# Kernel optimization log

Hardware: AMD Instinct MI355X
Metric: run time of the kernel (lower is better)

## Reference

```python
import jax, jax.numpy as jnp
import numpy as np

N, E, B = 100000, 1200000, 512
IN_DIM, HID, K, NCLS = 64, 64, 3, 10


def setup_inputs() -> dict:
    key = jax.random.key(0)
    ks = jax.random.split(key, 10)
    features = jax.random.normal(ks[0], (N, IN_DIM), jnp.float32)
    edge_src = jax.random.randint(ks[1], (E,), 0, N)
    edge_dst = jax.random.randint(ks[2], (E,), 0, N)
    graph_ids = jnp.sort(jax.random.randint(ks[3], (N,), 0, B))
    s1 = float(1.0 / np.sqrt(IN_DIM))
    W1 = jax.random.uniform(ks[4], (IN_DIM, HID), jnp.float32, -s1, s1)
    b1 = jnp.zeros((HID,), jnp.float32)
    s2 = float(1.0 / np.sqrt(HID))
    W2 = jax.random.uniform(ks[5], (HID, HID), jnp.float32, -s2, s2)
    b2 = jnp.zeros((HID,), jnp.float32)
    s3 = float(1.0 / np.sqrt(HID * 3))
    cw = jax.random.uniform(ks[6], (HID, HID, 3), jnp.float32, -s3, s3)
    cb = jax.random.uniform(ks[7], (HID,), jnp.float32, -s3, s3)
    Wc = jax.random.uniform(ks[8], (HID, NCLS), jnp.float32, -s2, s2)
    bc = jax.random.uniform(ks[9], (NCLS,), jnp.float32, -s2, s2)
    return dict(features=features, edge_src=edge_src, edge_dst=edge_dst,
                graph_ids=graph_ids, num_graphs=B,
                W1=W1, b1=b1, W2=W2, b2=b2, cw=cw, cb=cb, Wc=Wc, bc=bc)


def graph_conv(h, src, dst, W, b, n_nodes):
    # DGL GraphConv, norm='both', allow_zero_in_degree (degrees clamped to 1)
    ones = jnp.ones((src.shape[0],), h.dtype)
    out_deg = jnp.zeros((n_nodes,), h.dtype).at[src].add(ones)
    in_deg = jnp.zeros((n_nodes,), h.dtype).at[dst].add(ones)
    norm_s = jax.lax.rsqrt(jnp.clip(out_deg, 1.0, None))
    norm_d = jax.lax.rsqrt(jnp.clip(in_deg, 1.0, None))
    m = (h * norm_s[:, None]) @ W  # weight first; math identical to agg-first
    agg = jnp.zeros((n_nodes, W.shape[1]), h.dtype).at[dst].add(m[src])
    return agg * norm_d[:, None] + b


def sort_pool(h, gid, num_graphs, k):
    # DGL SortPooling: sort each node's features ascending along feature dim,
    # then take top-k nodes per graph by last feature value (descending),
    # zero-padding graphs with < k nodes. Output [num_graphs, k*D].
    hs = jnp.sort(h, axis=-1)
    key = hs[:, -1]
    order = jnp.lexsort((-key, gid))  # gid asc, key desc
    gid_s = gid[order]
    hs_s = hs[order]
    n = gid.shape[0]
    start = jnp.full((num_graphs,), n).at[gid_s].min(jnp.arange(n))
    rank = jnp.arange(n) - start[gid_s]  # within-graph rank by key desc
    mask = rank < k
    slot = gid_s * k + jnp.clip(rank, 0, k - 1)
    out = jnp.zeros((num_graphs * k, hs.shape[-1]), h.dtype).at[slot].add(
        jnp.where(mask[:, None], hs_s, jnp.zeros((), h.dtype)))
    return out.reshape(num_graphs, k * hs.shape[-1])


def reference(features, edge_src, edge_dst, graph_ids, num_graphs,
              W1, b1, W2, b2, cw, cb, Wc, bc):
    n = features.shape[0]
    h = jax.nn.relu(graph_conv(features, edge_src, edge_dst, W1, b1, n))
    h = jax.nn.relu(graph_conv(h, edge_src, edge_dst, W2, b2, n))
    p = sort_pool(h, graph_ids, num_graphs, K)          # [B, K*HID]
    x = p.reshape(num_graphs, HID, K)                    # faithful torch reshape
    # Conv1d(kernel=3, stride=1) on length-3 input -> length-1 output
    y = jax.nn.relu(jnp.einsum('bct,oct->bo', x, cw) + cb)
    return y @ Wc + bc
```

## Files before the change

### kernel.cpp

```cpp
#include <hip/hip_runtime.h>
#include <hip/hip_bf16.h>


#define PART_H 25088
#define HALF_H (PART_H / 2)
#define PART_F 12544
#define QUART_F (PART_F / 4)
#define MCH  64

__global__ void __launch_bounds__(256) k_histgemm(
    const int* __restrict__ esrc, const int* __restrict__ edst,
    unsigned char* __restrict__ hd, unsigned char* __restrict__ hs,
    const float* __restrict__ in, const float* __restrict__ W,
    float* __restrict__ mout, int N, int E, int PH, int histBlocks) {
  __shared__ float smem[12800];
  const int t = threadIdx.x;
  if (blockIdx.x < histBlocks) {
    unsigned int* lc = (unsigned int*)smem;
    const int b = blockIdx.x;
    const int half = PH * MCH;
    const int a = b / half;
    const int r = b % half;
    const int p = r % PH;
    const int m = r / PH;
    const int* __restrict__ arr = a ? esrc : edst;
    unsigned char* __restrict__ outp = a ? hs : hd;
    const int base = p * PART_H;
    const int lim = min(PART_H, N - base);
    for (int i = t; i < HALF_H; i += 256) lc[i] = 0u;
    __syncthreads();
    const long long cb = (long long)m * E / MCH;
    const long long ce = (long long)(m + 1) * E / MCH;
    const long long a0 = min((cb + 3) & ~3LL, ce);
    const long long nv = (ce - a0) >> 2;
    for (long long e = cb + t; e < a0; e += 256) {
      int d = arr[e] - base;
      if ((unsigned)d < (unsigned)lim) atomicAdd(&lc[d >> 1], 1u << ((d & 1) * 16));
    }
    const int4* __restrict__ a4p = (const int4*)(arr + a0);
    for (long long i = t; i < nv; i += 256) {
      int4 v4 = a4p[i];
      int d;
      d = v4.x - base; if ((unsigned)d < (unsigned)lim) atomicAdd(&lc[d >> 1], 1u << ((d & 1) * 16));
      d = v4.y - base; if ((unsigned)d < (unsigned)lim) atomicAdd(&lc[d >> 1], 1u << ((d & 1) * 16));
      d = v4.z - base; if ((unsigned)d < (unsigned)lim) atomicAdd(&lc[d >> 1], 1u << ((d & 1) * 16));
      d = v4.w - base; if ((unsigned)d < (unsigned)lim) atomicAdd(&lc[d >> 1], 1u << ((d & 1) * 16));
    }
    for (long long e = a0 + (nv << 2) + t; e < ce; e += 256) {
      int d = arr[e] - base;
      if ((unsigned)d < (unsigned)lim) atomicAdd(&lc[d >> 1], 1u << ((d & 1) * 16));
    }
    __syncthreads();
    unsigned char* slice = outp + ((size_t)p * MCH + m) * PART_H;
    for (int i = t; i < lim; i += 256)
      slice[i] = (unsigned char)((lc[i >> 1] >> ((i & 1) * 16)) & 0xffffu);
  } else {
    float* Wl = smem;
    float* Ac = smem + 4096;
    const int ch = (t & 7) * 8;
    const int nb = (t >> 3) * 4;
    for (int i = t; i < 1024; i += 256)
      ((float4*)Wl)[i] = ((const float4*)W)[i];
    const int gb = blockIdx.x - histBlocks;
    const int ng = gridDim.x - histBlocks;
    const int NT = (N + 127) >> 7;
    for (int tile = gb; tile < NT; tile += ng) {
      const int vbase = tile << 7;
      __syncthreads();
      for (int i = t; i < 2048; i += 256) {
        const int r = i >> 4;
        const int c = (i & 15) * 4;
        const int v = vbase + r;
        float4 val = make_float4(0.f, 0.f, 0.f, 0.f);
        if (v < N) val = *(const float4*)(in + (size_t)v * 64 + c);
        Ac[(c + 0) * 136 + r] = val.x;
        Ac[(c + 1) * 136 + r] = val.y;
        Ac[(c + 2) * 136 + r] = val.z;
        Ac[(c + 3) * 136 + r] = val.w;
      }
      __syncthreads();
      float acc[4][8];
#pragma unroll
      for (int j = 0; j < 4; ++j)
#pragma unroll
        for (int c = 0; c < 8; ++c) acc[j][c] = 0.f;
      for (int k = 0; k < 64; k += 4) {
#pragma unroll
        for (int kk = 0; kk < 4; ++kk) {
          const float4 aa = *(const float4*)&Ac[(k + kk) * 136 + nb];
          const float4 w0 = *(const float4*)&Wl[(k + kk) * 64 + ch];
          const float4 w1 = *(const float4*)&Wl[(k + kk) * 64 + ch + 4];
          const float an[4] = {aa.x, aa.y, aa.z, aa.w};
          const float wn[8] = {w0.x, w0.y, w0.z, w0.w, w1.x, w1.y, w1.z, w1.w};
#pragma unroll
          for (int j = 0; j < 4; ++j)
#pragma unroll
            for (int c = 0; c < 8; ++c)
              acc[j][c] = fmaf(an[j], wn[c], acc[j][c]);
        }
      }
#pragma unroll
      for (int j = 0; j < 4; ++j) {
        const int v = vbase + nb + j;
        if (v < N) {
          float4 o0, o1;
          o0.x = acc[j][0]; o0.y = acc[j][1]; o0.z = acc[j][2]; o0.w = acc[j][3];
          o1.x = acc[j][4]; o1.y = acc[j][5]; o1.z = acc[j][6]; o1.w = acc[j][7];
          *(float4*)(mout + (size_t)v * 64 + ch)     = o0;
          *(float4*)(mout + (size_t)v * 64 + ch + 4) = o1;
        }
      }
    }
  }
}

__global__ void k_off(unsigned char* __restrict__ hd, const unsigned char* __restrict__ hs,
                      int* __restrict__ deg_d, float* __restrict__ norm_s,
                      float* __restrict__ norm_d, int N) {
  int v = blockIdx.x * blockDim.x + threadIdx.x;
  if (v >= N) return;
  size_t base = (size_t)(v / PART_H) * MCH * PART_H + (v % PART_H);
  int run = 0;
#pragma unroll
  for (int m = 0; m < MCH; ++m) {
    int t = hd[base + (size_t)m * PART_H];
    hd[base + (size_t)m * PART_H] = (unsigned char)run;
    run += t;
  }
  int s = 0;
#pragma unroll
  for (int m = 0; m < MCH; ++m) s += hs[base + (size_t)m * PART_H];
  deg_d[v] = run;
  norm_d[v] = rsqrtf((float)max(run, 1));
  norm_s[v] = rsqrtf((float)max(s, 1));
}

__global__ void k_scan1(const int* __restrict__ deg, int* __restrict__ rowptr,
                        int* __restrict__ bsum, int N) {
  __shared__ int sums[256];
  const int t = threadIdx.x;
  const int base = blockIdx.x * 2048 + t * 8;
  int loc[8];
  int tot = 0;
#pragma unroll
  for (int j = 0; j < 8; ++j) {
    int idx = base + j;
    loc[j] = tot;
    tot += (idx < N) ? deg[idx] : 0;
  }
  sums[t] = tot;
  __syncthreads();
  for (int off = 1; off < 256; off <<= 1) {
    int x = (t >= off) ? sums[t - off] : 0;
    __syncthreads();
    sums[t] += x;
    __syncthreads();
  }
  int excl = (t == 0) ? 0 : sums[t - 1];
#pragma unroll
  for (int j = 0; j < 8; ++j) {
    int idx = base + j;
    if (idx < N) rowptr[idx] = excl + loc[j];
  }
  if (t == 255) bsum[blockIdx.x] = sums[255];
}

__global__ void k_scan2(int* __restrict__ bsum, int nb) {
  int lane = threadIdx.x;
  int v = (lane < nb) ? bsum[lane] : 0;
  int inc = v;
#pragma unroll
  for (int off = 1; off < 64; off <<= 1) {
    int o = __shfl_up(inc, off, 64);
    if (lane >= off) inc += o;
  }
  if (lane < nb) bsum[lane] = inc - v;
}

__global__ void k_scan3(int* __restrict__ rowptr, const int* __restrict__ bsum, int N) {
  int v = blockIdx.x * blockDim.x + threadIdx.x;
  if (v < N) rowptr[v] += bsum[v >> 11];
}

__global__ void k_fill2(const int* __restrict__ esrc, const int* __restrict__ edst,
                        const unsigned char* __restrict__ hd, const int* __restrict__ rowptr,
                        int* __restrict__ csr, int N, int E, int PF) {
  __shared__ unsigned int cur4[QUART_F];
  const int b = blockIdx.x;
  const int p = b % PF;
  const int m = b / PF;
  const int base = p * PART_F;
  const int lim = min(PART_F, N - base);
  const unsigned char* slice = hd + ((size_t)(p >> 1) * MCH + m) * PART_H
                                  + (size_t)(p & 1) * PART_F;
  const unsigned int* slice4 = (const unsigned int*)slice;
  for (int i = threadIdx.x; i < QUART_F; i += blockDim.x) cur4[i] = slice4[i];
  __syncthreads();
  const int* __restrict__ rp = rowptr + base;
  const long long cb = (long long)m * E / MCH;
  const long long ce = (long long)(m + 1) * E / MCH;
  const long long a0 = min((cb + 3) & ~3LL, ce);
  const long long nv = (ce - a0) >> 2;
  for (long long e = cb + threadIdx.x; e < a0; e += blockDim.x) {
    int d = edst[e] - base;
    if ((unsigned)d < (unsigned)lim) {
      unsigned int old = atomicAdd(&cur4[d >> 2], 1u << ((d & 3) * 8));
      csr[rp[d] + ((old >> ((d & 3) * 8)) & 0xff)] = esrc[e];
    }
  }
  const int4* __restrict__ d4p = (const int4*)(edst + a0);
  const int4* __restrict__ s4p = (const int4*)(esrc + a0);
  for (long long i = threadIdx.x; i < nv; i += blockDim.x) {
    int4 d4 = d4p[i];
    int4 s4 = s4p[i];
    int d;
    d = d4.x - base;
    if ((unsigned)d < (unsigned)lim) {
      unsigned int old = atomicAdd(&cur4[d >> 2], 1u << ((d & 3) * 8));
      csr[rp[d] + ((old >> ((d & 3) * 8)) & 0xff)] = s4.x;
    }
    d = d4.y - base;
    if ((unsigned)d < (unsigned)lim) {
      unsigned int old = atomicAdd(&cur4[d >> 2], 1u << ((d & 3) * 8));
      csr[rp[d] + ((old >> ((d & 3) * 8)) & 0xff)] = s4.y;
    }
    d = d4.z - base;
    if ((unsigned)d < (unsigned)lim) {
      unsigned int old = atomicAdd(&cur4[d >> 2], 1u << ((d & 3) * 8));
      csr[rp[d] + ((old >> ((d & 3) * 8)) & 0xff)] = s4.z;
    }
    d = d4.w - base;
    if ((unsigned)d < (unsigned)lim) {
      unsigned int old = atomicAdd(&cur4[d >> 2], 1u << ((d & 3) * 8));
      csr[rp[d] + ((old >> ((d & 3) * 8)) & 0xff)] = s4.w;
    }
  }
  for (long long e = a0 + (nv << 2) + threadIdx.x; e < ce; e += blockDim.x) {
    int d = edst[e] - base;
    if ((unsigned)d < (unsigned)lim) {
      unsigned int old = atomicAdd(&cur4[d >> 2], 1u << ((d & 3) * 8));
      csr[rp[d] + ((old >> ((d & 3) * 8)) & 0xff)] = esrc[e];
    }
  }
}

__global__ void __launch_bounds__(256) k_gemm64(
    const float* __restrict__ in, const float* __restrict__ norm,
    const float* __restrict__ W, float* __restrict__ out, int N) {
  __shared__ float Wl[4096];
  __shared__ float Ac[64 * 136];
  const int t = threadIdx.x;
  const int ch = (t & 7) * 8;
  const int nb = (t >> 3) * 4;
  for (int i = t; i < 1024; i += 256)
    ((float4*)Wl)[i] = ((const float4*)W)[i];
  const int NT = (N + 127) >> 7;
  for (int tile = blockIdx.x; tile < NT; tile += gridDim.x) {
    const int vbase = tile << 7;
    __syncthreads();
    for (int i = t; i < 2048; i += 256) {
      const int r = i >> 4;
      const int c = (i & 15) * 4;
      const int v = vbase + r;
      float4 val = make_float4(0.f, 0.f, 0.f, 0.f);
      if (v < N) val = *(const float4*)(in + (size_t)v * 64 + c);
      Ac[(c + 0) * 136 + r] = val.x;
      Ac[(c + 1) * 136 + r] = val.y;
      Ac[(c + 2) * 136 + r] = val.z;
      Ac[(c + 3) * 136 + r] = val.w;
    }
    __syncthreads();
    float acc[4][8];
#pragma unroll
    for (int j = 0; j < 4; ++j)
#pragma unroll
      for (int c = 0; c < 8; ++c) acc[j][c] = 0.f;
    for (int k = 0; k < 64; k += 4) {
#pragma unroll
      for (int kk = 0; kk < 4; ++kk) {
        const float4 aa = *(const float4*)&Ac[(k + kk) * 136 + nb];
        const float4 w0 = *(const float4*)&Wl[(k + kk) * 64 + ch];
        const float4 w1 = *(const float4*)&Wl[(k + kk) * 64 + ch + 4];
        const float an[4] = {aa.x, aa.y, aa.z, aa.w};
        const float wn[8] = {w0.x, w0.y, w0.z, w0.w, w1.x, w1.y, w1.z, w1.w};
#pragma unroll
        for (int j = 0; j < 4; ++j)
#pragma unroll
          for (int c = 0; c < 8; ++c)
            acc[j][c] = fmaf(an[j], wn[c], acc[j][c]);
      }
    }
#pragma unroll
    for (int j = 0; j < 4; ++j) {
      const int v = vbase + nb + j;
      if (v < N) {
        const float nm = norm[v];
        float4 o0, o1;
        o0.x = acc[j][0] * nm; o0.y = acc[j][1] * nm;
        o0.z = acc[j][2] * nm; o0.w = acc[j][3] * nm;
        o1.x = acc[j][4] * nm; o1.y = acc[j][5] * nm;
        o1.z = acc[j][6] * nm; o1.w = acc[j][7] * nm;
        *(float4*)(out + (size_t)v * 64 + ch)     = o0;
        *(float4*)(out + (size_t)v * 64 + ch + 4) = o1;
      }
    }
  }
}

__global__ void k_gather(const float* __restrict__ m, const int* __restrict__ rowptr,
                         const int* __restrict__ deg, const float* __restrict__ norm_d,
                         const float* __restrict__ bias, const int* __restrict__ csr,
                         const float* __restrict__ nsrc,
                         const int* __restrict__ gid, int* __restrict__ gstart,
                         float* __restrict__ h, float* __restrict__ key, int N) {
  const int w = blockIdx.x * (blockDim.x >> 6) + (threadIdx.x >> 6);
  if (w >= N) return;
  const int lane = threadIdx.x & 63;
  const int quad = lane & 15;
  const int grp = lane >> 4;
  if (gid != nullptr && lane == 0) {
    int g = gid[w];
    if (w == 0 || gid[w - 1] != g) gstart[g] = w;
  }
  const int start = rowptr[w];
  const int cnt = deg[w];
  float4 acc0 = make_float4(0.f, 0.f, 0.f, 0.f);
  float4 acc1 = make_float4(0.f, 0.f, 0.f, 0.f);
  int i = grp;
  if (nsrc != nullptr) {
    for (; i + 4 < cnt; i += 8) {
      int s0 = csr[start + i];
      int s1 = csr[start + i + 4];
      float n0 = nsrc[s0], n1 = nsrc[s1];
      const float4 v0 = *(const float4*)(m + (size_t)s0 * 64 + quad * 4);
      const float4 v1 = *(const float4*)(m + (size_t)s1 * 64 + quad * 4);
      acc0.x = fmaf(v0.x, n0, acc0.x); acc0.y = fmaf(v0.y, n0, acc0.y);
      acc0.z = fmaf(v0.z, n0, acc0.z); acc0.w = fmaf(v0.w, n0, acc0.w);
      acc1.x = fmaf(v1.x, n1, acc1.x); acc1.y = fmaf(v1.y, n1, acc1.y);
      acc1.z = fmaf(v1.z, n1, acc1.z); acc1.w = fmaf(v1.w, n1, acc1.w);
    }
    if (i < cnt) {
      int s0 = csr[start + i];
      float n0 = nsrc[s0];
      const float4 v0 = *(const float4*)(m + (size_t)s0 * 64 + quad * 4);
      acc0.x = fmaf(v0.x, n0, acc0.x); acc0.y = fmaf(v0.y, n0, acc0.y);
      acc0.z = fmaf(v0.z, n0, acc0.z); acc0.w = fmaf(v0.w, n0, acc0.w);
    }
  } else {
    for (; i + 4 < cnt; i += 8) {
      int s0 = csr[start + i];
      int s1 = csr[start + i + 4];
      const float4 v0 = *(const float4*)(m + (size_t)s0 * 64 + quad * 4);
      const float4 v1 = *(const float4*)(m + (size_t)s1 * 64 + quad * 4);
      acc0.x += v0.x; acc0.y += v0.y; acc0.z += v0.z; acc0.w += v0.w;
      acc1.x += v1.x; acc1.y += v1.y; acc1.z += v1.z; acc1.w += v1.w;
    }
    if (i < cnt) {
      int s0 = csr[start + i];
      const float4 v0 = *(const float4*)(m + (size_t)s0 * 64 + quad * 4);
      acc0.x += v0.x; acc0.y += v0.y; acc0.z += v0.z; acc0.w += v0.w;
    }
  }
  acc0.x += acc1.x; acc0.y += acc1.y; acc0.z += acc1.z; acc0.w += acc1.w;
#pragma unroll
  for (int off = 16; off <= 32; off <<= 1) {
    acc0.x += __shfl_xor(acc0.x, off, 64);
    acc0.y += __shfl_xor(acc0.y, off, 64);
    acc0.z += __shfl_xor(acc0.z, off, 64);
    acc0.w += __shfl_xor(acc0.w, off, 64);
  }
  const float nd = norm_d[w];
  const float4 bq = *(const float4*)(bias + quad * 4);
  float4 o;
  o.x = fmaxf(fmaf(acc0.x, nd, bq.x), 0.f);
  o.y = fmaxf(fmaf(acc0.y, nd, bq.y), 0.f);
  o.z = fmaxf(fmaf(acc0.z, nd, bq.z), 0.f);
  o.w = fmaxf(fmaf(acc0.w, nd, bq.w), 0.f);
  if (grp == 0) *(float4*)(h + (size_t)w * 64 + quad * 4) = o;
  if (key != nullptr) {
    float mx = fmaxf(fmaxf(o.x, o.y), fmaxf(o.z, o.w));
#pragma unroll
    for (int off = 1; off < 16; off <<= 1) mx = fmaxf(mx, __shfl_xor(mx, off, 64));
    if (lane == 0) key[w] = mx;
  }
}

__global__ void k_bfin(const int* __restrict__ gstart, int* __restrict__ gcnt,
                       int B, int N) {
  __shared__ int sm[512];
  const int g = threadIdx.x;
  sm[g] = (g < B) ? gstart[g] : 0x7fffffff;
  __syncthreads();
  for (int off = 1; off < 512; off <<= 1) {
    int x = (g + off < 512) ? sm[g + off] : 0x7fffffff;
    __syncthreads();
    sm[g] = min(sm[g], x);
    __syncthreads();
  }
  if (g < B) {
    int gs = gstart[g];
    int ns = (g + 1 < 512) ? min(sm[g + 1], N) : N;
    gcnt[g] = (gs < N) ? (ns - gs) : 0;
  }
}

__global__ void __launch_bounds__(256) k_tail(
    const float* __restrict__ key, const int* __restrict__ gstart,
    const int* __restrict__ gcnt, const float* __restrict__ h,
    const float* __restrict__ cw, const float* __restrict__ cb,
    const float* __restrict__ Wc, const float* __restrict__ bc,
    float* __restrict__ out, int B, int N) {
  __shared__ int sel[3];
  __shared__ float prow[192];
  const int b = blockIdx.x;
  const int wid = threadIdx.x >> 6;
  const int lane = threadIdx.x & 63;

  if (wid == 0) {
    const int s = gstart[b], c = gcnt[b];
    float v0 = -1.f, v1 = -1.f, v2 = -1.f;
    int i0 = 0x7fffffff, i1 = 0x7fffffff, i2 = 0x7fffffff;
    for (int i = s + lane; i < s + c; i += 64) {
      float kv = key[i];
      if (kv > v0 || (kv == v0 && i < i0)) {
        v2 = v1; i2 = i1; v1 = v0; i1 = i0; v0 = kv; i0 = i;
      } else if (kv > v1 || (kv == v1 && i < i1)) {
        v2 = v1; i2 = i1; v1 = kv; i1 = i;
      } else if (kv > v2 || (kv == v2 && i < i2)) {
        v2 = kv; i2 = i;
      }
    }
    int ptr = 0;
    for (int r = 0; r < 3; ++r) {
      float mv = (ptr == 0) ? v0 : (ptr == 1) ? v1 : (ptr == 2) ? v2 : -1.f;
      int   mi = (ptr == 0) ? i0 : (ptr == 1) ? i1 : (ptr == 2) ? i2 : 0x7fffffff;
      float bv = mv; int bi = mi;
#pragma unroll
      for (int off = 32; off; off >>= 1) {
        float ov = __shfl_xor(bv, off, 64);
        int   oi = __shfl_xor(bi, off, 64);
        if (ov > bv || (ov == bv && oi < bi)) { bv = ov; bi = oi; }
      }
      if (bi == mi && ptr < 3) ptr++;
      if (lane == 0) sel[r] = (bi == 0x7fffffff) ? -1 : bi;
    }
  }
  __syncthreads();
  if (wid < 3) {
    int node = sel[wid];
    float v = 0.f;
    if (node >= 0) {
      v = h[(size_t)node * 64 + lane];
      for (int k2 = 2; k2 <= 64; k2 <<= 1) {
        for (int j = k2 >> 1; j > 0; j >>= 1) {
          float o = __shfl_xor(v, j, 64);
          bool up = ((lane & k2) == 0);
          bool lower = ((lane & j) == 0);
          v = (lower == up) ? fminf(v, o) : fmaxf(v, o);
        }
      }
    }
    prow[wid * 64 + lane] = v;
  }
  __syncthreads();
  if (wid == 0) {
    float y = cb[lane];
    for (int j = 0; j < 192; ++j) y = fmaf(prow[j], cw[lane * 192 + j], y);
    float ry = fmaxf(y, 0.f);
    for (int c = 0; c < 10; ++c) {
      float s = ry * Wc[lane * 10 + c];
#pragma unroll
      for (int off = 32; off; off >>= 1) s += __shfl_xor(s, off, 64);
      if (lane == 0) out[b * 10 + c] = s + bc[c];
    }
  }
}

extern "C" void kernel_launch(void* const* d_in, const int* in_sizes, int n_in,
                              void* d_out, int out_size, void* d_ws, size_t ws_size,
                              hipStream_t stream) {
  const float* features = (const float*)d_in[0];
  const int*   esrc     = (const int*)d_in[1];
  const int*   edst     = (const int*)d_in[2];
  const int*   gid      = (const int*)d_in[3];
  const float* W1 = (const float*)d_in[5];
  const float* b1 = (const float*)d_in[6];
  const float* W2 = (const float*)d_in[7];
  const float* b2 = (const float*)d_in[8];
  const float* cw = (const float*)d_in[9];
  const float* cb = (const float*)d_in[10];
  const float* Wc = (const float*)d_in[11];
  const float* bc = (const float*)d_in[12];
  float* out = (float*)d_out;

  const int N = in_sizes[0] / 64;
  const int E = in_sizes[1];
  const int B = out_size / 10;
  const size_t N64 = (size_t)N * 64;
  const int nscan = (N + 2047) / 2048;
  const int PH = (N + PART_H - 1) / PART_H;
  const int PF = (N + PART_F - 1) / PART_F;
  const size_t HSZ = (size_t)PH * MCH * PART_H;
  const int NT = (N + 127) / 128;
  const int histBlocks = 2 * PH * MCH;

  float* bufA   = (float*)d_ws;
  float* bufB   = bufA + N64;
  int*   deg_d  = (int*)(bufB + N64);
  float* norm_s = (float*)(deg_d + N);
  float* norm_d = norm_s + N;
  float* key    = norm_d + N;
  int*   rowptr = (int*)(key + N);
  int*   csr    = rowptr + N;
  int*   bsum   = csr + E;
  int*   gstart = bsum + 64;
  int*   gcnt   = gstart + B;
  unsigned char* hd = (unsigned char*)(gcnt + B);
  unsigned char* hs = hd + HSZ;

  const int TB = 256;

  hipMemsetAsync(gstart, 0x7f, (size_t)B * sizeof(int), stream);

  k_histgemm<<<histBlocks + NT, TB, 0, stream>>>(esrc, edst, hd, hs,
                                                 features, W1, bufA,
                                                 N, E, PH, histBlocks);
  k_off<<<(N + TB - 1) / TB, TB, 0, stream>>>(hd, hs, deg_d, norm_s, norm_d, N);
  k_scan1<<<nscan, 256, 0, stream>>>(deg_d, rowptr, bsum, N);
  k_scan2<<<1, 64, 0, stream>>>(bsum, nscan);
  k_scan3<<<(N + TB - 1) / TB, TB, 0, stream>>>(rowptr, bsum, N);
  k_fill2<<<PF * MCH, TB, 0, stream>>>(esrc, edst, hd, rowptr, csr, N, E, PF);

  k_gather<<<(N + 3) / 4, TB, 0, stream>>>(bufA, rowptr, deg_d, norm_d, b1, csr,
                                           norm_s, nullptr, nullptr,
                                           bufB, nullptr, N);

  k_gemm64<<<NT, TB, 0, stream>>>(bufB, norm_s, W2, bufA, N);
  k_gather<<<(N + 3) / 4, TB, 0, stream>>>(bufA, rowptr, deg_d, norm_d, b2, csr,
                                           nullptr, gid, gstart,
                                           bufB, key, N);

  k_bfin<<<1, 512, 0, stream>>>(gstart, gcnt, B, N);
  k_tail<<<B, TB, 0, stream>>>(key, gstart, gcnt, bufB, cw, cb, Wc, bc, out, B, N);
}
```

Baseline: 307.1 us.

## Pack histogram counters into bytes and widen the gather to 8 rows per wave

The degree histogram now packs four 8-bit counters per shared-memory word instead of two 16-bit ones. That doubles the partition size, so fewer histogram blocks, and fewer passes over the edge arrays, are needed. The gather kernel now gives 8 lanes of 64 channels each to every neighbour row, with two float4 loads per lane. This keeps 8 neighbour rows (16 when unrolled) in flight per wavefront instead of 4, at the cost of more registers and an extra shuffle stage. The 8-bit counters overflow if more than 255 edges from one chunk hit the same node, but the output was already stored as bytes.

```diff
diff --git a/kernel.cpp b/kernel.cpp
--- a/kernel.cpp
+++ b/kernel.cpp
@@ -2,9 +2,9 @@
 #include <hip/hip_bf16.h>
 
 
-#define PART_H 25088
-#define HALF_H (PART_H / 2)
-#define PART_F 12544
+#define PART_H 50176
+#define QPART_H (PART_H / 4)
+#define PART_F 25088
 #define QUART_F (PART_F / 4)
 #define MCH  64
 
@@ -27,7 +27,7 @@
     unsigned char* __restrict__ outp = a ? hs : hd;
     const int base = p * PART_H;
     const int lim = min(PART_H, N - base);
-    for (int i = t; i < HALF_H; i += 256) lc[i] = 0u;
+    for (int i = t; i < QPART_H; i += 256) lc[i] = 0u;
     __syncthreads();
     const long long cb = (long long)m * E / MCH;
     const long long ce = (long long)(m + 1) * E / MCH;
@@ -35,25 +35,25 @@
     const long long nv = (ce - a0) >> 2;
     for (long long e = cb + t; e < a0; e += 256) {
       int d = arr[e] - base;
-      if ((unsigned)d < (unsigned)lim) atomicAdd(&lc[d >> 1], 1u << ((d & 1) * 16));
+      if ((unsigned)d < (unsigned)lim) atomicAdd(&lc[d >> 2], 1u << ((d & 3) * 8));
     }
     const int4* __restrict__ a4p = (const int4*)(arr + a0);
     for (long long i = t; i < nv; i += 256) {
       int4 v4 = a4p[i];
       int d;
-      d = v4.x - base; if ((unsigned)d < (unsigned)lim) atomicAdd(&lc[d >> 1], 1u << ((d & 1) * 16));
-      d = v4.y - base; if ((unsigned)d < (unsigned)lim) atomicAdd(&lc[d >> 1], 1u << ((d & 1) * 16));
-      d = v4.z - base; if ((unsigned)d < (unsigned)lim) atomicAdd(&lc[d >> 1], 1u << ((d & 1) * 16));
-      d = v4.w - base; if ((unsigned)d < (unsigned)lim) atomicAdd(&lc[d >> 1], 1u << ((d & 1) * 16));
+      d = v4.x - base; if ((unsigned)d < (unsigned)lim) atomicAdd(&lc[d >> 2], 1u << ((d & 3) * 8));
+      d = v4.y - base; if ((unsigned)d < (unsigned)lim) atomicAdd(&lc[d >> 2], 1u << ((d & 3) * 8));
+      d = v4.z - base; if ((unsigned)d < (unsigned)lim) atomicAdd(&lc[d >> 2], 1u << ((d & 3) * 8));
+      d = v4.w - base; if ((unsigned)d < (unsigned)lim) atomicAdd(&lc[d >> 2], 1u << ((d & 3) * 8));
     }
     for (long long e = a0 + (nv << 2) + t; e < ce; e += 256) {
       int d = arr[e] - base;
-      if ((unsigned)d < (unsigned)lim) atomicAdd(&lc[d >> 1], 1u << ((d & 1) * 16));
+      if ((unsigned)d < (unsigned)lim) atomicAdd(&lc[d >> 2], 1u << ((d & 3) * 8));
     }
     __syncthreads();
     unsigned char* slice = outp + ((size_t)p * MCH + m) * PART_H;
     for (int i = t; i < lim; i += 256)
-      slice[i] = (unsigned char)((lc[i >> 1] >> ((i & 1) * 16)) & 0xffffu);
+      slice[i] = (unsigned char)((lc[i >> 2] >> ((i & 3) * 8)) & 0xffu);
   } else {
     float* Wl = smem;
     float* Ac = smem + 4096;
@@ -316,71 +316,108 @@
   const int w = blockIdx.x * (blockDim.x >> 6) + (threadIdx.x >> 6);
   if (w >= N) return;
   const int lane = threadIdx.x & 63;
-  const int quad = lane & 15;
-  const int grp = lane >> 4;
+  const int chb = (lane & 7) * 8;
+  const int grp = lane >> 3;
   if (gid != nullptr && lane == 0) {
     int g = gid[w];
     if (w == 0 || gid[w - 1] != g) gstart[g] = w;
   }
   const int start = rowptr[w];
   const int cnt = deg[w];
-  float4 acc0 = make_float4(0.f, 0.f, 0.f, 0.f);
-  float4 acc1 = make_float4(0.f, 0.f, 0.f, 0.f);
+  float4 a00 = make_float4(0.f, 0.f, 0.f, 0.f);
+  float4 a01 = make_float4(0.f, 0.f, 0.f, 0.f);
+  float4 a10 = make_float4(0.f, 0.f, 0.f, 0.f);
+  float4 a11 = make_float4(0.f, 0.f, 0.f, 0.f);
   int i = grp;
   if (nsrc != nullptr) {
-    for (; i + 4 < cnt; i += 8) {
+    for (; i + 8 < cnt; i += 16) {
       int s0 = csr[start + i];
-      int s1 = csr[start + i + 4];
+      int s1 = csr[start + i + 8];
       float n0 = nsrc[s0], n1 = nsrc[s1];
-      const float4 v0 = *(const float4*)(m + (size_t)s0 * 64 + quad * 4);
-      const float4 v1 = *(const float4*)(m + (size_t)s1 * 64 + quad * 4);
-      acc0.x = fmaf(v0.x, n0, acc0.x); acc0.y = fmaf(v0.y, n0, acc0.y);
-      acc0.z = fmaf(v0.z, n0, acc0.z); acc0.w = fmaf(v0.w, n0, acc0.w);
-      acc1.x = fmaf(v1.x, n1, acc1.x); acc1.y = fmaf(v1.y, n1, acc1.y);
-      acc1.z = fmaf(v1.z, n1, acc1.z); acc1.w = fmaf(v1.w, n1, acc1.w);
+      const float* r0 = m + (size_t)s0 * 64 + chb;
+      const float* r1 = m + (size_t)s1 * 64 + chb;
+      const float4 v00 = *(const float4*)r0;
+      const float4 v01 = *(const float4*)(r0 + 4);
+      const float4 v10 = *(const float4*)r1;
+      const float4 v11 = *(const float4*)(r1 + 4);
+      a00.x = fmaf(v00.x, n0, a00.x); a00.y = fmaf(v00.y, n0, a00.y);
+      a00.z = fmaf(v00.z, n0, a00.z); a00.w = fmaf(v00.w, n0, a00.w);
+      a01.x = fmaf(v01.x, n0, a01.x); a01.y = fmaf(v01.y, n0, a01.y);
+      a01.z = fmaf(v01.z, n0, a01.z); a01.w = fmaf(v01.w, n0, a01.w);
+      a10.x = fmaf(v10.x, n1, a10.x); a10.y = fmaf(v10.y, n1, a10.y);
+      a10.z = fmaf(v10.z, n1, a10.z); a10.w = fmaf(v10.w, n1, a10.w);
+      a11.x = fmaf(v11.x, n1, a11.x); a11.y = fmaf(v11.y, n1, a11.y);
+      a11.z = fmaf(v11.z, n1, a11.z); a11.w = fmaf(v11.w, n1, a11.w);
     }
     if (i < cnt) {
       int s0 = csr[start + i];
       float n0 = nsrc[s0];
-      const float4 v0 = *(const float4*)(m + (size_t)s0 * 64 + quad * 4);
-      acc0.x = fmaf(v0.x, n0, acc0.x); acc0.y = fmaf(v0.y, n0, acc0.y);
-      acc0.z = fmaf(v0.z, n0, acc0.z); acc0.w = fmaf(v0.w, n0, acc0.w);
+      const float* r0 = m + (size_t)s0 * 64 + chb;
+      const float4 v00 = *(const float4*)r0;
+      const float4 v01 = *(const float4*)(r0 + 4);
+      a00.x = fmaf(v00.x, n0, a00.x); a00.y = fmaf(v00.y, n0, a00.y);
+      a00.z = fmaf(v00.z, n0, a00.z); a00.w = fmaf(v00.w, n0, a00.w);
+      a01.x = fmaf(v01.x, n0, a01.x); a01.y = fmaf(v01.y, n0, a01.y);
+      a01.z = fmaf(v01.z, n0, a01.z); a01.w = fmaf(v01.w, n0, a01.w);
     }
   } else {
-    for (; i + 4 < cnt; i += 8) {
+    for (; i + 8 < cnt; i += 16) {
       int s0 = csr[start + i];
-      int s1 = csr[start + i + 4];
-      const float4 v0 = *(const float4*)(m + (size_t)s0 * 64 + quad * 4);
-      const float4 v1 = *(const float4*)(m + (size_t)s1 * 64 + quad * 4);
-      acc0.x += v0.x; acc0.y += v0.y; acc0.z += v0.z; acc0.w += v0.w;
-      acc1.x += v1.x; acc1.y += v1.y; acc1.z += v1.z; acc1.w += v1.w;
+      int s1 = csr[start + i + 8];
+      const float* r0 = m + (size_t)s0 * 64 + chb;
+      const float* r1 = m + (size_t)s1 * 64 + chb;
+      const float4 v00 = *(const float4*)r0;
+      const float4 v01 = *(const float4*)(r0 + 4);
+      const float4 v10 = *(const float4*)r1;
+      const float4 v11 = *(const float4*)(r1 + 4);
+      a00.x += v00.x; a00.y += v00.y; a00.z += v00.z; a00.w += v00.w;
+      a01.x += v01.x; a01.y += v01.y; a01.z += v01.z; a01.w += v01.w;
+      a10.x += v10.x; a10.y += v10.y; a10.z += v10.z; a10.w += v10.w;
+      a11.x += v11.x; a11.y += v11.y; a11.z += v11.z; a11.w += v11.w;
     }
     if (i < cnt) {
       int s0 = csr[start + i];
-      const float4 v0 = *(const float4*)(m + (size_t)s0 * 64 + quad * 4);
-      acc0.x += v0.x; acc0.y += v0.y; acc0.z += v0.z; acc0.w += v0.w;
-    }
-  }
-  acc0.x += acc1.x; acc0.y += acc1.y; acc0.z += acc1.z; acc0.w += acc1.w;
-#pragma unroll
-  for (int off = 16; off <= 32; off <<= 1) {
-    acc0.x += __shfl_xor(acc0.x, off, 64);
-    acc0.y += __shfl_xor(acc0.y, off, 64);
-    acc0.z += __shfl_xor(acc0.z, off, 64);
-    acc0.w += __shfl_xor(acc0.w, off, 64);
+      const float* r0 = m + (size_t)s0 * 64 + chb;
+      const float4 v00 = *(const float4*)r0;
+      const float4 v01 = *(const float4*)(r0 + 4);
+      a00.x += v00.x; a00.y += v00.y; a00.z += v00.z; a00.w += v00.w;
+      a01.x += v01.x; a01.y += v01.y; a01.z += v01.z; a01.w += v01.w;
+    }
+  }
+  a00.x += a10.x; a00.y += a10.y; a00.z += a10.z; a00.w += a10.w;
+  a01.x += a11.x; a01.y += a11.y; a01.z += a11.z; a01.w += a11.w;
+#pragma unroll
+  for (int off = 8; off <= 32; off <<= 1) {
+    a00.x += __shfl_xor(a00.x, off, 64);
+    a00.y += __shfl_xor(a00.y, off, 64);
+    a00.z += __shfl_xor(a00.z, off, 64);
+    a00.w += __shfl_xor(a00.w, off, 64);
+    a01.x += __shfl_xor(a01.x, off, 64);
+    a01.y += __shfl_xor(a01.y, off, 64);
+    a01.z += __shfl_xor(a01.z, off, 64);
+    a01.w += __shfl_xor(a01.w, off, 64);
   }
   const float nd = norm_d[w];
-  const float4 bq = *(const float4*)(bias + quad * 4);
-  float4 o;
-  o.x = fmaxf(fmaf(acc0.x, nd, bq.x), 0.f);
-  o.y = fmaxf(fmaf(acc0.y, nd, bq.y), 0.f);
-  o.z = fmaxf(fmaf(acc0.z, nd, bq.z), 0.f);
-  o.w = fmaxf(fmaf(acc0.w, nd, bq.w), 0.f);
-  if (grp == 0) *(float4*)(h + (size_t)w * 64 + quad * 4) = o;
+  const float4 b0 = *(const float4*)(bias + chb);
+  const float4 b1 = *(const float4*)(bias + chb + 4);
+  float4 o0, o1;
+  o0.x = fmaxf(fmaf(a00.x, nd, b0.x), 0.f);
+  o0.y = fmaxf(fmaf(a00.y, nd, b0.y), 0.f);
+  o0.z = fmaxf(fmaf(a00.z, nd, b0.z), 0.f);
+  o0.w = fmaxf(fmaf(a00.w, nd, b0.w), 0.f);
+  o1.x = fmaxf(fmaf(a01.x, nd, b1.x), 0.f);
+  o1.y = fmaxf(fmaf(a01.y, nd, b1.y), 0.f);
+  o1.z = fmaxf(fmaf(a01.z, nd, b1.z), 0.f);
+  o1.w = fmaxf(fmaf(a01.w, nd, b1.w), 0.f);
+  if (grp == 0) {
+    *(float4*)(h + (size_t)w * 64 + chb)     = o0;
+    *(float4*)(h + (size_t)w * 64 + chb + 4) = o1;
+  }
   if (key != nullptr) {
-    float mx = fmaxf(fmaxf(o.x, o.y), fmaxf(o.z, o.w));
-#pragma unroll
-    for (int off = 1; off < 16; off <<= 1) mx = fmaxf(mx, __shfl_xor(mx, off, 64));
+    float mx = fmaxf(fmaxf(fmaxf(o0.x, o0.y), fmaxf(o0.z, o0.w)),
+                     fmaxf(fmaxf(o1.x, o1.y), fmaxf(o1.z, o1.w)));
+#pragma unroll
+    for (int off = 1; off < 8; off <<= 1) mx = fmaxf(mx, __shfl_xor(mx, off, 64));
     if (lane == 0) key[w] = mx;
   }
 }
```

Result: no change. 302.9 us (-1.4%).
